# Performance work log

Measured on AMD Instinct MI355X. Metric: run time of the kernel, lower is better.

Reference implementation:

```python
import jax, jax.numpy as jnp
import numpy as np

B, H, W, C, F = 8, 128, 128, 256, 256

def setup_inputs() -> dict:
    key = jax.random.key(0)
    k1, k2, k3 = jax.random.split(key, 3)
    x = jax.random.normal(k1, (B, H, W, C), dtype=jnp.float32)
    style = jax.random.normal(k2, (B, 1, 1, C), dtype=jnp.float32)
    # he_uniform over fan_in = 3*3*C
    limit = np.sqrt(6.0 / (3 * 3 * C)).astype(np.float32)
    kernel = jax.random.uniform(k3, (3, 3, C, F), dtype=jnp.float32, minval=-limit, maxval=limit)
    return {"x": x, "style": style, "kernel": kernel}

def reference(x, style, kernel):
    b, h, w_, c = x.shape
    f = kernel.shape[-1]
    # per-sample modulation: [B,1,1,C,1] * [1,3,3,C,F] -> [B,3,3,C,F]
    wmod = kernel[None] * (style[..., None] + 1.0)
    demod = jnp.sqrt(jnp.sum(jnp.square(wmod), axis=(1, 2, 3), keepdims=True) + 1e-8)
    wmod = wmod / demod
    # grouped conv trick: x -> [1, B*C, H, W], filters -> [3,3,C,B*F], groups=B
    xg = jnp.transpose(x, (0, 3, 1, 2)).reshape(1, b * c, h, w_)
    wf = jnp.transpose(wmod, (1, 2, 3, 0, 4)).reshape(3, 3, c, b * f)
    y = jax.lax.conv_general_dilated(
        xg, wf, window_strides=(1, 1), padding='SAME',
        dimension_numbers=('NCHW', 'HWIO', 'NCHW'),
        feature_group_count=b)
    y = y.reshape(b, f, h, w_)
    return jnp.transpose(y, (0, 2, 3, 1))
```

## Files before the change

kernel.cpp:

```cpp
#include <hip/hip_runtime.h>
#include <hip/hip_bf16.h>


#define NB 8
#define NH 128
#define NW 128
#define NC 256
#define NF 256

typedef __attribute__((ext_vector_type(8))) short bf16x8;
typedef __attribute__((ext_vector_type(4))) float f32x4;

__device__ __forceinline__ void gload16(const ushort* g, ushort* l) {
    __builtin_amdgcn_global_load_lds(
        (const __attribute__((address_space(1))) unsigned int*)g,
        (__attribute__((address_space(3))) unsigned int*)l, 16, 0, 0);
}

__global__ void k_cvt(const float* __restrict__ x, ushort* __restrict__ xbf) {
    int i = (blockIdx.x * blockDim.x + threadIdx.x) * 4;
    float4 v = *(const float4*)(x + i);
    union { ushort4 u; __hip_bfloat16 h[4]; } o;
    o.h[0] = __float2bfloat16(v.x);
    o.h[1] = __float2bfloat16(v.y);
    o.h[2] = __float2bfloat16(v.z);
    o.h[3] = __float2bfloat16(v.w);
    *(ushort4*)(xbf + i) = o.u;
}

__global__ void k_modw(const float* __restrict__ kern, const float* __restrict__ style,
                       ushort* __restrict__ wm) {
    int b = blockIdx.x >> 8;
    int f = blockIdx.x & 255;
    int c = threadIdx.x;
    float s = style[b * 256 + c] + 1.0f;
    float w[9];
    float acc = 0.f;
#pragma unroll
    for (int t = 0; t < 9; ++t) {
        w[t] = kern[(t * 256 + c) * 256 + f] * s;
        acc += w[t] * w[t];
    }
#pragma unroll
    for (int off = 32; off; off >>= 1) acc += __shfl_down(acc, off);
    __shared__ float part[4];
    if ((threadIdx.x & 63) == 0) part[threadIdx.x >> 6] = acc;
    __syncthreads();
    float total = part[0] + part[1] + part[2] + part[3];
    float inv = 1.0f / sqrtf(total + 1e-8f);
#pragma unroll
    for (int t = 0; t < 9; ++t) {
        union { ushort u; __hip_bfloat16 h; } o;
        o.h = __float2bfloat16(w[t] * inv);
        wm[(((b * 9 + t) * 256 + f) * 256) + c] = o.u;
    }
}

__global__ void __launch_bounds__(256, 2)
k_conv(const ushort* __restrict__ xbf, const ushort* __restrict__ wm,
       float* __restrict__ out) {
    const int bidx = (blockIdx.x & 7) * 128 + (blockIdx.x >> 3);
    const int h = bidx & 127;
    const int b = bidx >> 7;

    __shared__ ushort As[3][130 * 32];
    __shared__ ushort Bs[3][256 * 32];

    const int tid = threadIdx.x;
    const int wave = tid >> 6, lane = tid & 63;
    const int wm_ = wave & 1, wn_ = wave >> 1;
    const int lrow = lane & 15;
    const int quad = lane >> 4;
    const int lw = lane >> 2;
    const int lc = (lane & 3) * 8;

    for (int i = tid; i < 3 * 2 * 32; i += 256) {
        int dh = i >> 6;
        int side = (i >> 5) & 1;
        int cc = i & 31;
        As[dh][(side ? 129 : 0) * 32 + cc] = 0;
    }
#pragma unroll
    for (int dh = 0; dh < 3; ++dh) {
        int hp = h + dh - 1;
        if (hp < 0 || hp >= 128) {
            for (int i = tid; i < 130 * 32; i += 256) As[dh][i] = 0;
        }
    }

    f32x4 acc[4][8];
    const f32x4 zero4 = {0.f, 0.f, 0.f, 0.f};
#pragma unroll
    for (int mi = 0; mi < 4; ++mi)
#pragma unroll
        for (int ni = 0; ni < 8; ++ni) acc[mi][ni] = zero4;

    const ushort* wmb = wm + (size_t)b * 9 * 65536;

    auto stageA = [&](int c0) {
#pragma unroll
        for (int dh = 0; dh < 3; ++dh) {
            int hp = h + dh - 1;
            if (hp >= 0 && hp < 128) {
                const ushort* src = xbf + ((size_t)(b * 128 + hp) * 128) * 256 + c0;
#pragma unroll
                for (int j = 0; j < 2; ++j) {
                    int w = j * 64 + wave * 16;
                    gload16(src + (w + lw) * 256 + lc, &As[dh][(w + 1) * 32]);
                }
            }
        }
    };
    auto stageB = [&](int c0, int tap, int buf) {
        const ushort* src = wmb + tap * 65536 + c0;
#pragma unroll
        for (int j = 0; j < 4; ++j) {
            int fl = j * 64 + wave * 16;
            gload16(src + (fl + lw) * 256 + lc, &Bs[buf][fl * 32]);
        }
    };

    bf16x8 af[4];
    bf16x8 bfr[2][8];

    stageA(0);
    stageB(0, 0, 0);
    stageB(0, 1, 1);

    for (int ci = 0; ci < 8; ++ci) {
        const int c0 = ci * 32;
        __syncthreads();
#pragma unroll
        for (int ni = 0; ni < 8; ++ni) {
            int fl = wn_ * 128 + ni * 16 + lrow;
            bfr[0][ni] = *(const bf16x8*)&Bs[0][fl * 32 + quad * 8];
        }
#pragma unroll
        for (int t = 0; t < 9; ++t) {
            if (t > 0) __syncthreads();
            if (t < 7) stageB(c0, t + 2, (t + 2) % 3);
            const int dh = t / 3, dw = t % 3;
#pragma unroll
            for (int mi = 0; mi < 4; ++mi) {
                int w = wm_ * 64 + mi * 16 + lrow;
                af[mi] = *(const bf16x8*)&As[dh][(w + dw) * 32 + quad * 8];
            }
            if (t < 8) {
#pragma unroll
                for (int ni = 0; ni < 8; ++ni) {
                    int fl = wn_ * 128 + ni * 16 + lrow;
                    bfr[(t + 1) & 1][ni] =
                        *(const bf16x8*)&Bs[(t + 1) % 3][fl * 32 + quad * 8];
                }
            }
#pragma unroll
            for (int mi = 0; mi < 4; ++mi)
#pragma unroll
                for (int ni = 0; ni < 8; ++ni)
                    acc[mi][ni] = __builtin_amdgcn_mfma_f32_16x16x32_bf16(
                        af[mi], bfr[t & 1][ni], acc[mi][ni], 0, 0, 0);
        }
        __syncthreads();
        if (ci < 7) {
            stageA(c0 + 32);
            stageB(c0 + 32, 0, 0);
            stageB(c0 + 32, 1, 1);
        }
    }

    float* obase = out + ((size_t)(b * 128 + h) * 128) * 256;
#pragma unroll
    for (int mi = 0; mi < 4; ++mi) {
        int wrow = wm_ * 64 + mi * 16 + quad * 4;
#pragma unroll
        for (int ni = 0; ni < 8; ++ni) {
            int f = wn_ * 128 + ni * 16 + lrow;
            f32x4 v = acc[mi][ni];
#pragma unroll
            for (int r = 0; r < 4; ++r) {
                obase[(wrow + r) * 256 + f] = v[r];
            }
        }
    }
}

extern "C" void kernel_launch(void* const* d_in, const int* in_sizes, int n_in,
                              void* d_out, int out_size, void* d_ws, size_t ws_size,
                              hipStream_t stream) {
    const float* x     = (const float*)d_in[0];
    const float* style = (const float*)d_in[1];
    const float* kern  = (const float*)d_in[2];
    float* out = (float*)d_out;

    ushort* xbf = (ushort*)d_ws;
    ushort* wmod = xbf + (size_t)NB * NH * NW * NC;

    k_cvt<<<(NB * NH * NW * NC) / (256 * 4), 256, 0, stream>>>(x, xbf);
    k_modw<<<NB * NF, 256, 0, stream>>>(kern, style, wmod);
    k_conv<<<NB * NH, 256, 0, stream>>>(xbf, wmod, out);
}
```

Baseline: 373.8 us.

## Load weight fragments directly from global into registers and double-buffer activation tiles

Removes the LDS staging of the modulated weights: each wave now loads its B fragments straight from global/L2 into registers one tap ahead. The activation tile in LDS is double-buffered across channel chunks, so the next chunk's rows are prefetched while the current chunk computes, which drops most of the per-tap barriers. This trades LDS traffic and synchronisation for more global/L2 load pressure and exposed global latency on the weight path.

```diff
diff --git a/kernel.cpp b/kernel.cpp
--- a/kernel.cpp
+++ b/kernel.cpp
@@ -63,8 +63,7 @@
     const int h = bidx & 127;
     const int b = bidx >> 7;
 
-    __shared__ ushort As[3][130 * 32];
-    __shared__ ushort Bs[3][256 * 32];
+    __shared__ ushort As[2][3][130 * 32];
 
     const int tid = threadIdx.x;
     const int wave = tid >> 6, lane = tid & 63;
@@ -74,17 +73,23 @@
     const int lw = lane >> 2;
     const int lc = (lane & 3) * 8;
 
-    for (int i = tid; i < 3 * 2 * 32; i += 256) {
-        int dh = i >> 6;
-        int side = (i >> 5) & 1;
-        int cc = i & 31;
-        As[dh][(side ? 129 : 0) * 32 + cc] = 0;
+#pragma unroll
+    for (int p = 0; p < 2; ++p) {
+        if (tid < 3 * 2 * 32) {
+            int dh = tid >> 6;
+            int side = (tid >> 5) & 1;
+            int cc = tid & 31;
+            As[p][dh][(side ? 129 : 0) * 32 + cc] = 0;
+        }
     }
 #pragma unroll
     for (int dh = 0; dh < 3; ++dh) {
         int hp = h + dh - 1;
         if (hp < 0 || hp >= 128) {
-            for (int i = tid; i < 130 * 32; i += 256) As[dh][i] = 0;
+            for (int i = tid; i < 130 * 32; i += 256) {
+                As[0][dh][i] = 0;
+                As[1][dh][i] = 0;
+            }
         }
     }
 
@@ -96,8 +101,9 @@
         for (int ni = 0; ni < 8; ++ni) acc[mi][ni] = zero4;
 
     const ushort* wmb = wm + (size_t)b * 9 * 65536;
+    const ushort* wrow = wmb + (wn_ * 128 + lrow) * 256 + quad * 8;
 
-    auto stageA = [&](int c0) {
+    auto stageA = [&](int c0, int p) {
 #pragma unroll
         for (int dh = 0; dh < 3; ++dh) {
             int hp = h + dh - 1;
@@ -106,79 +112,68 @@
 #pragma unroll
                 for (int j = 0; j < 2; ++j) {
                     int w = j * 64 + wave * 16;
-                    gload16(src + (w + lw) * 256 + lc, &As[dh][(w + 1) * 32]);
+                    gload16(src + (w + lw) * 256 + lc, &As[p][dh][(w + 1) * 32]);
                 }
             }
-        }
-    };
-    auto stageB = [&](int c0, int tap, int buf) {
-        const ushort* src = wmb + tap * 65536 + c0;
-#pragma unroll
-        for (int j = 0; j < 4; ++j) {
-            int fl = j * 64 + wave * 16;
-            gload16(src + (fl + lw) * 256 + lc, &Bs[buf][fl * 32]);
         }
     };
 
     bf16x8 af[4];
     bf16x8 bfr[2][8];
 
-    stageA(0);
-    stageB(0, 0, 0);
-    stageB(0, 1, 1);
+    stageA(0, 0);
+#pragma unroll
+    for (int ni = 0; ni < 8; ++ni)
+        bfr[0][ni] = *(const bf16x8*)(wrow + ni * 4096);
 
-    for (int ci = 0; ci < 8; ++ci) {
-        const int c0 = ci * 32;
-        __syncthreads();
+    for (int ci2 = 0; ci2 < 4; ++ci2) {
 #pragma unroll
-        for (int ni = 0; ni < 8; ++ni) {
-            int fl = wn_ * 128 + ni * 16 + lrow;
-            bfr[0][ni] = *(const bf16x8*)&Bs[0][fl * 32 + quad * 8];
-        }
+        for (int half = 0; half < 2; ++half) {
+            const int ci = 2 * ci2 + half;
+            const int c0 = ci * 32;
+            __syncthreads();
+            if (ci < 7) stageA(c0 + 32, half ^ 1);
 #pragma unroll
-        for (int t = 0; t < 9; ++t) {
-            if (t > 0) __syncthreads();
-            if (t < 7) stageB(c0, t + 2, (t + 2) % 3);
-            const int dh = t / 3, dw = t % 3;
+            for (int t = 0; t < 9; ++t) {
+                const int par = (half + t) & 1;
+                if (t < 8) {
+                    const ushort* src = wrow + (t + 1) * 65536 + c0;
 #pragma unroll
-            for (int mi = 0; mi < 4; ++mi) {
-                int w = wm_ * 64 + mi * 16 + lrow;
-                af[mi] = *(const bf16x8*)&As[dh][(w + dw) * 32 + quad * 8];
+                    for (int ni = 0; ni < 8; ++ni)
+                        bfr[par ^ 1][ni] = *(const bf16x8*)(src + ni * 4096);
+                } else if (ci < 7) {
+                    const ushort* src = wrow + (c0 + 32);
+#pragma unroll
+                    for (int ni = 0; ni < 8; ++ni)
+                        bfr[par ^ 1][ni] = *(const bf16x8*)(src + ni * 4096);
+                }
+                const int dh = t / 3, dw = t % 3;
+#pragma unroll
+                for (int mi = 0; mi < 4; ++mi) {
+                    int w = wm_ * 64 + mi * 16 + lrow;
+                    af[mi] = *(const bf16x8*)&As[half][dh][(w + dw) * 32 + quad * 8];
+                }
+#pragma unroll
+                for (int mi = 0; mi < 4; ++mi)
+#pragma unroll
+                    for (int ni = 0; ni < 8; ++ni)
+                        acc[mi][ni] = __builtin_amdgcn_mfma_f32_16x16x32_bf16(
+                            af[mi], bfr[par][ni], acc[mi][ni], 0, 0, 0);
             }
-            if (t < 8) {
-#pragma unroll
-                for (int ni = 0; ni < 8; ++ni) {
-                    int fl = wn_ * 128 + ni * 16 + lrow;
-                    bfr[(t + 1) & 1][ni] =
-                        *(const bf16x8*)&Bs[(t + 1) % 3][fl * 32 + quad * 8];
-                }
-            }
-#pragma unroll
-            for (int mi = 0; mi < 4; ++mi)
-#pragma unroll
-                for (int ni = 0; ni < 8; ++ni)
-                    acc[mi][ni] = __builtin_amdgcn_mfma_f32_16x16x32_bf16(
-                        af[mi], bfr[t & 1][ni], acc[mi][ni], 0, 0, 0);
-        }
-        __syncthreads();
-        if (ci < 7) {
-            stageA(c0 + 32);
-            stageB(c0 + 32, 0, 0);
-            stageB(c0 + 32, 1, 1);
         }
     }
 
     float* obase = out + ((size_t)(b * 128 + h) * 128) * 256;
 #pragma unroll
     for (int mi = 0; mi < 4; ++mi) {
-        int wrow = wm_ * 64 + mi * 16 + quad * 4;
+        int wrow_ = wm_ * 64 + mi * 16 + quad * 4;
 #pragma unroll
         for (int ni = 0; ni < 8; ++ni) {
             int f = wn_ * 128 + ni * 16 + lrow;
             f32x4 v = acc[mi][ni];
 #pragma unroll
             for (int r = 0; r < 4; ++r) {
-                obase[(wrow + r) * 256 + f] = v[r];
+                obase[(wrow_ + r) * 256 + f] = v[r];
             }
         }
     }
```

Result: slower. 546.2 us (+46.1%).
